# Kernel optimization log

Hardware: AMD Instinct MI355X
Metric: run time of the kernel (lower is better)

Reference implementation:

```python
import jax, jax.numpy as jnp
import numpy as np

EMBED = 1024
HEADS = 16
HEAD_DIM = EMBED // HEADS

def setup_inputs() -> dict:
    key = jax.random.key(0)
    k1, k2, k3, k4, k5 = jax.random.split(key, 5)
    scale = 1.0 / np.sqrt(EMBED)
    return {
        "x": jax.random.normal(k1, (4, 2048, EMBED), dtype=jnp.float32),
        "qkv_w": jax.random.uniform(k2, (3 * EMBED, EMBED), minval=-scale, maxval=scale, dtype=jnp.float32),
        "qkv_b": jax.random.uniform(k3, (3 * EMBED,), minval=-scale, maxval=scale, dtype=jnp.float32),
        "out_w": jax.random.uniform(k4, (EMBED, EMBED), minval=-scale, maxval=scale, dtype=jnp.float32),
        "out_b": jax.random.uniform(k5, (EMBED,), minval=-scale, maxval=scale, dtype=jnp.float32),
    }

def reference(x, qkv_w, qkv_b, out_w, out_b):
    b, n, _ = x.shape
    # torch Linear: x @ W.T + b
    qkv = (jnp.einsum('bne,fe->bnf', x, qkv_w) + qkv_b).reshape(b, n, 3, HEADS, HEAD_DIM)
    q, k, v = qkv[:, :, 0], qkv[:, :, 1], qkv[:, :, 2]
    scores = jnp.einsum('bnhd,bmhd->bhnm', q, k) / jnp.sqrt(jnp.float32(HEAD_DIM))
    attn = jax.nn.softmax(scores, axis=-1)  # dropout p=0.0 -> identity
    out = jnp.einsum('bhnm,bmhd->bnhd', attn, v).reshape(b, n, EMBED)
    return jnp.einsum('bne,fe->bnf', out, out_w) + out_b
```

## Files before the change

### kernel.cpp

```cpp
#include <hip/hip_runtime.h>
#include <hip/hip_bf16.h>

typedef __bf16 bf16;
typedef __attribute__((ext_vector_type(8))) __bf16 bf16x8;
typedef __attribute__((ext_vector_type(4))) __bf16 bf16x4;
typedef __attribute__((ext_vector_type(4))) float f32x4;
typedef __attribute__((ext_vector_type(16))) float f32x16;

#define EMBED 1024
#define HEADS 16
#define HD 64
#define NB 4
#define SEQ 2048
#define TOK (NB * SEQ)
#define F3 (3 * EMBED)

#define QSCALE 0.18033688011112042f
#define CEXP 16.0f

__device__ __forceinline__ float exp2_hw(float x) {
  float r;
  asm("v_exp_f32 %0, %1" : "=v"(r) : "v"(x));
  return r;
}

__device__ __forceinline__ unsigned int cvtpk_bf16(float lo, float hi) {
  unsigned int r;
  asm("v_cvt_pk_bf16_f32 %0, %1, %2" : "=v"(r) : "v"(lo), "v"(hi));
  return r;
}

__device__ __forceinline__ void gload_lds16(const void* g, void* l) {
  __builtin_amdgcn_global_load_lds(
      (const __attribute__((address_space(1))) unsigned int*)(unsigned long long)g,
      (__attribute__((address_space(3))) unsigned int*)(unsigned int)(unsigned long long)l,
      16, 0, 0);
}

__global__ void cvt_bf16_kernel(const float* __restrict__ in, bf16* __restrict__ out, int n4) {
  int i = blockIdx.x * blockDim.x + threadIdx.x;
  if (i < n4) {
    float4 v = ((const float4*)in)[i];
    bf16x4 o;
    o[0] = (bf16)v.x; o[1] = (bf16)v.y; o[2] = (bf16)v.z; o[3] = (bf16)v.w;
    ((bf16x4*)out)[i] = o;
  }
}

template <int MODE, typename OUT_T>
__global__ __launch_bounds__(256) void gemm_bt(const bf16* __restrict__ A,
                                               const bf16* __restrict__ Bw,
                                               const float* __restrict__ bias,
                                               OUT_T* __restrict__ C,
                                               bf16* __restrict__ VT,
                                               int K, int Ncols) {
  __shared__ __align__(16) bf16 As[2][128 * 32];
  __shared__ __align__(16) bf16 Bs[2][128 * 32];

  const int tid = threadIdx.x;
  const int lane = tid & 63;
  const int w = tid >> 6;
  const int wr = w >> 1, wc = w & 1;
  const int lr = lane & 15, lg = lane >> 4;

  const int r0 = tid >> 2;
  const int csw = ((tid & 3) ^ ((tid >> 3) & 3)) * 8;
  const bf16* Ag = A + (size_t)blockIdx.x * 128 * K + (size_t)r0 * K + csw;
  const bf16* Bg = Bw + (size_t)blockIdx.y * 128 * K + (size_t)r0 * K + csw;

  f32x4 acc[4][4] = {};
  const int co = (lg ^ ((lr >> 1) & 3)) * 8;
  const int ntiles = K >> 5;

#define GSTAGE(buf)                                      \
  do {                                                   \
    gload_lds16(Ag, &As[buf][tid * 8]);                  \
    gload_lds16(Ag + 64 * K, &As[buf][(tid + 256) * 8]); \
    gload_lds16(Bg, &Bs[buf][tid * 8]);                  \
    gload_lds16(Bg + 64 * K, &Bs[buf][(tid + 256) * 8]); \
    Ag += 32; Bg += 32;                                  \
  } while (0)

  GSTAGE(0);
  __syncthreads();

  for (int t = 0; t < ntiles; ++t) {
    const int cur = t & 1;
    if (t + 1 < ntiles) GSTAGE(cur ^ 1);

    bf16x8 af[4], bfr[4];
#pragma unroll
    for (int mi = 0; mi < 4; ++mi)
      af[mi] = *(const bf16x8*)&As[cur][(wr * 64 + mi * 16 + lr) * 32 + co];
#pragma unroll
    for (int ni = 0; ni < 4; ++ni)
      bfr[ni] = *(const bf16x8*)&Bs[cur][(wc * 64 + ni * 16 + lr) * 32 + co];

#pragma unroll
    for (int mi = 0; mi < 4; ++mi)
#pragma unroll
      for (int ni = 0; ni < 4; ++ni)
        acc[mi][ni] = __builtin_amdgcn_mfma_f32_16x16x32_bf16(af[mi], bfr[ni], acc[mi][ni], 0, 0, 0);

    __syncthreads();
  }
#undef GSTAGE

  const int rowb = blockIdx.x * 128 + wr * 64;
  const int colb = blockIdx.y * 128 + wc * 64;

  if (MODE == 1 && blockIdx.y >= 16) {
#pragma unroll
    for (int ni = 0; ni < 4; ++ni) {
      int col = colb + ni * 16 + lr;
      int fc = col - 2 * EMBED;
      int hh = fc >> 6, d = fc & 63;
      float bv = bias[col];
#pragma unroll
      for (int mi = 0; mi < 4; ++mi) {
        int row = rowb + mi * 16 + lg * 4;
        int bb = row >> 11, nn = row & 2047;
        bf16x4 pk;
#pragma unroll
        for (int j = 0; j < 4; ++j) pk[j] = (bf16)(acc[mi][ni][j] + bv);
        *(bf16x4*)&VT[((size_t)((bb * HEADS + hh) * HD + d)) * SEQ + nn] = pk;
      }
    }
  } else {
    const float scale = (MODE == 1 && blockIdx.y < 8) ? QSCALE : 1.0f;
#pragma unroll
    for (int ni = 0; ni < 4; ++ni) {
      int col = colb + ni * 16 + lr;
      float bv = bias[col];
#pragma unroll
      for (int mi = 0; mi < 4; ++mi) {
#pragma unroll
        for (int j = 0; j < 4; ++j) {
          int row = rowb + mi * 16 + lg * 4 + j;
          C[(size_t)row * Ncols + col] = (OUT_T)((acc[mi][ni][j] + bv) * scale);
        }
      }
    }
  }
}

__global__ __launch_bounds__(256, 4) void attn_fwd(const bf16* __restrict__ QK,
                                                   const bf16* __restrict__ VT,
                                                   bf16* __restrict__ O) {
  __shared__ __align__(16) bf16 Kb[2][64 * 64];
  __shared__ __align__(16) bf16 Vb[2][64 * 64];
  __shared__ float Lrow[4][32];

  const int qb = blockIdx.x, h = blockIdx.y, b = blockIdx.z;
  const int tid = threadIdx.x, lane = tid & 63, w = tid >> 6;
  const int lq = lane & 31, hi = lane >> 5;
  const int sw = lq & 7;

  bf16x8 qf[4];
  {
    const bf16* qp = QK + (size_t)(b * SEQ + qb * 128 + w * 32 + lq) * 2048 + h * HD + hi * 8;
#pragma unroll
    for (int c = 0; c < 4; ++c) qf[c] = *(const bf16x8*)(qp + c * 16);
  }

  const int rk = tid >> 3;
  const int cc = ((tid & 7) ^ (rk & 7)) * 8;
  const bf16* kp = QK + (size_t)(b * SEQ + rk) * 2048 + EMBED + h * HD + cc;
  const bf16* vp = VT + ((size_t)((b * HEADS + h) * HD + rk)) * SEQ + cc;

  f32x16 oacc[2] = {};
  float lp = 0.f;
  f32x16 cinit;
#pragma unroll
  for (int r = 0; r < 16; ++r) cinit[r] = -CEXP;

#define ASTAGE(buf)                                         \
  do {                                                      \
    gload_lds16(kp, &Kb[buf][tid * 8]);                     \
    gload_lds16(kp + 32 * 2048, &Kb[buf][(tid + 256) * 8]); \
    gload_lds16(vp, &Vb[buf][tid * 8]);                     \
    gload_lds16(vp + 32 * SEQ, &Vb[buf][(tid + 256) * 8]);  \
    kp += (size_t)64 * 2048; vp += 64;                      \
  } while (0)

  ASTAGE(0);
  __syncthreads();

  for (int t = 0; t < SEQ / 64; ++t) {
    const bf16* Kc = Kb[t & 1];
    const bf16* Vc = Vb[t & 1];
    if (t + 1 < SEQ / 64) ASTAGE((t & 1) ^ 1);

    f32x16 s0 = cinit, s1 = cinit;
    __builtin_amdgcn_s_setprio(1);
#pragma unroll
    for (int c = 0; c < 4; ++c) {
      const int cg = ((c * 2 + hi) ^ sw) * 8;
      bf16x8 kf0 = *(const bf16x8*)&Kc[lq * 64 + cg];
      bf16x8 kf1 = *(const bf16x8*)&Kc[(32 + lq) * 64 + cg];
      s0 = __builtin_amdgcn_mfma_f32_32x32x16_bf16(kf0, qf[c], s0, 0, 0, 0);
      s1 = __builtin_amdgcn_mfma_f32_32x32x16_bf16(kf1, qf[c], s1, 0, 0, 0);
    }
    __builtin_amdgcn_s_setprio(0);

    bf16x8 pa[4];
#pragma unroll
    for (int g = 0; g < 2; ++g) {
      const f32x16& sv = g ? s1 : s0;
      float pv[16];
#pragma unroll
      for (int r = 0; r < 16; ++r) { pv[r] = exp2_hw(sv[r]); lp += pv[r]; }
#pragma unroll
      for (int cidx = 0; cidx < 2; ++cidx) {
        const int pb = cidx * 8;
        unsigned int x0 = cvtpk_bf16(pv[pb + 0], pv[pb + 1]);
        unsigned int y0 = cvtpk_bf16(pv[pb + 4], pv[pb + 5]);
        unsigned int x1 = cvtpk_bf16(pv[pb + 2], pv[pb + 3]);
        unsigned int y1 = cvtpk_bf16(pv[pb + 6], pv[pb + 7]);
        auto r0 = __builtin_amdgcn_permlane32_swap(x0, y0, false, false);
        auto r1 = __builtin_amdgcn_permlane32_swap(x1, y1, false, false);
        union { unsigned int u[4]; bf16x8 v; } fr;
        fr.u[0] = r0[0]; fr.u[1] = r1[0]; fr.u[2] = r0[1]; fr.u[3] = r1[1];
        pa[g * 2 + cidx] = fr.v;
      }
    }

    __builtin_amdgcn_s_setprio(1);
#pragma unroll
    for (int k4 = 0; k4 < 4; ++k4) {
      const int cg = ((k4 * 2 + hi) ^ sw) * 8;
      bf16x8 vf0 = *(const bf16x8*)&Vc[lq * 64 + cg];
      bf16x8 vf1 = *(const bf16x8*)&Vc[(32 + lq) * 64 + cg];
      oacc[0] = __builtin_amdgcn_mfma_f32_32x32x16_bf16(pa[k4], vf0, oacc[0], 0, 0, 0);
      oacc[1] = __builtin_amdgcn_mfma_f32_32x32x16_bf16(pa[k4], vf1, oacc[1], 0, 0, 0);
    }
    __builtin_amdgcn_s_setprio(0);

    __syncthreads();
  }
#undef ASTAGE

  float lsum = lp + __shfl_xor(lp, 32, 64);
  if (hi == 0) Lrow[w][lq] = 1.0f / lsum;
  asm volatile("s_waitcnt lgkmcnt(0)" ::: "memory");

  const size_t obase = (size_t)(b * SEQ + qb * 128 + w * 32) * EMBED + h * HD + lq;
#pragma unroll
  for (int r = 0; r < 16; ++r) {
    const int qr = (r & 3) + 8 * (r >> 2) + 4 * hi;
    const float rl = Lrow[w][qr];
    O[obase + (size_t)qr * EMBED]      = (bf16)(oacc[0][r] * rl);
    O[obase + (size_t)qr * EMBED + 32] = (bf16)(oacc[1][r] * rl);
  }
}

extern "C" void kernel_launch(void* const* d_in, const int* in_sizes, int n_in,
                              void* d_out, int out_size, void* d_ws, size_t ws_size,
                              hipStream_t stream) {
  const float* x     = (const float*)d_in[0];
  const float* qkv_w = (const float*)d_in[1];
  const float* qkv_b = (const float*)d_in[2];
  const float* out_w = (const float*)d_in[3];
  const float* out_b = (const float*)d_in[4];
  float* out = (float*)d_out;

  char* ws = (char*)d_ws;
  bf16* xb    = (bf16*)(ws);
  bf16* wqb   = (bf16*)(ws + 16777216);
  bf16* wob   = (bf16*)(ws + 23068672);
  bf16* qk    = (bf16*)(ws + 25165824);
  bf16* vT    = (bf16*)(ws + 58720256);
  bf16* attno = (bf16*)(ws + 75497472);

  cvt_bf16_kernel<<<(TOK * EMBED / 4 + 255) / 256, 256, 0, stream>>>(x, xb, TOK * EMBED / 4);
  cvt_bf16_kernel<<<(F3 * EMBED / 4 + 255) / 256, 256, 0, stream>>>(qkv_w, wqb, F3 * EMBED / 4);
  cvt_bf16_kernel<<<(EMBED * EMBED / 4 + 255) / 256, 256, 0, stream>>>(out_w, wob, EMBED * EMBED / 4);

  gemm_bt<1, bf16><<<dim3(TOK / 128, F3 / 128), 256, 0, stream>>>(xb, wqb, qkv_b, qk, vT, EMBED, 2048);

  attn_fwd<<<dim3(SEQ / 128, HEADS, NB), 256, 0, stream>>>(qk, vT, attno);

  gemm_bt<0, float><<<dim3(TOK / 128, EMBED / 128), 256, 0, stream>>>(attno, wob, out_b, out, nullptr, EMBED, EMBED);
}
```

Baseline: 273.6 us.

## Process 256 queries per attention block with 64 rows per wave

Each wave of the attention kernel now handles two 32-row query groups, so every K and V tile staged in LDS and read into registers feeds twice as many MFMAs. The grid is halved to 512 blocks on a 1D launch, and the block index is remapped so that blocks with the same (batch, head) land on different XCDs or are spread in a particular order. Register pressure doubles for the accumulators, and launch bounds drop to 2 blocks per CU to fit. The fixed offset of the softmax exponent is unchanged.

```diff
diff --git a/kernel.cpp b/kernel.cpp
--- a/kernel.cpp
+++ b/kernel.cpp
@@ -144,23 +144,29 @@
   }
 }
 
-__global__ __launch_bounds__(256, 4) void attn_fwd(const bf16* __restrict__ QK,
+__global__ __launch_bounds__(256, 2) void attn_fwd(const bf16* __restrict__ QK,
                                                    const bf16* __restrict__ VT,
                                                    bf16* __restrict__ O) {
   __shared__ __align__(16) bf16 Kb[2][64 * 64];
   __shared__ __align__(16) bf16 Vb[2][64 * 64];
-  __shared__ float Lrow[4][32];
-
-  const int qb = blockIdx.x, h = blockIdx.y, b = blockIdx.z;
+  __shared__ float Lrow[4][64];
+
+  const int orig = blockIdx.x;
+  const int wid = ((orig & 7) << 6) | (orig >> 3);
+  const int qb = wid & 7;
+  const int g = wid >> 3;
+  const int h = g & 15, b = g >> 4;
+
   const int tid = threadIdx.x, lane = tid & 63, w = tid >> 6;
   const int lq = lane & 31, hi = lane >> 5;
   const int sw = lq & 7;
 
-  bf16x8 qf[4];
-  {
-    const bf16* qp = QK + (size_t)(b * SEQ + qb * 128 + w * 32 + lq) * 2048 + h * HD + hi * 8;
-#pragma unroll
-    for (int c = 0; c < 4; ++c) qf[c] = *(const bf16x8*)(qp + c * 16);
+  bf16x8 qf[2][4];
+#pragma unroll
+  for (int grp = 0; grp < 2; ++grp) {
+    const bf16* qp = QK + (size_t)(b * SEQ + qb * 256 + w * 64 + grp * 32 + lq) * 2048 + h * HD + hi * 8;
+#pragma unroll
+    for (int c = 0; c < 4; ++c) qf[grp][c] = *(const bf16x8*)(qp + c * 16);
   }
 
   const int rk = tid >> 3;
@@ -168,8 +174,8 @@
   const bf16* kp = QK + (size_t)(b * SEQ + rk) * 2048 + EMBED + h * HD + cc;
   const bf16* vp = VT + ((size_t)((b * HEADS + h) * HD + rk)) * SEQ + cc;
 
-  f32x16 oacc[2] = {};
-  float lp = 0.f;
+  f32x16 oacc[2][2] = {};
+  float lp0 = 0.f, lp1 = 0.f;
   f32x16 cinit;
 #pragma unroll
   for (int r = 0; r < 16; ++r) cinit[r] = -CEXP;
@@ -183,6 +189,25 @@
     kp += (size_t)64 * 2048; vp += 64;                      \
   } while (0)
 
+  auto packP = [&](const f32x16& sv, float& lpacc, bf16x8* pa) {
+    float pv[16];
+#pragma unroll
+    for (int r = 0; r < 16; ++r) { pv[r] = exp2_hw(sv[r]); lpacc += pv[r]; }
+#pragma unroll
+    for (int cidx = 0; cidx < 2; ++cidx) {
+      const int pb = cidx * 8;
+      unsigned int x0 = cvtpk_bf16(pv[pb + 0], pv[pb + 1]);
+      unsigned int y0 = cvtpk_bf16(pv[pb + 4], pv[pb + 5]);
+      unsigned int x1 = cvtpk_bf16(pv[pb + 2], pv[pb + 3]);
+      unsigned int y1 = cvtpk_bf16(pv[pb + 6], pv[pb + 7]);
+      auto r0 = __builtin_amdgcn_permlane32_swap(x0, y0, false, false);
+      auto r1 = __builtin_amdgcn_permlane32_swap(x1, y1, false, false);
+      union { unsigned int u[4]; bf16x8 v; } fr;
+      fr.u[0] = r0[0]; fr.u[1] = r1[0]; fr.u[2] = r0[1]; fr.u[3] = r1[1];
+      pa[cidx] = fr.v;
+    }
+  };
+
   ASTAGE(0);
   __syncthreads();
 
@@ -191,66 +216,61 @@
     const bf16* Vc = Vb[t & 1];
     if (t + 1 < SEQ / 64) ASTAGE((t & 1) ^ 1);
 
-    f32x16 s0 = cinit, s1 = cinit;
-    __builtin_amdgcn_s_setprio(1);
-#pragma unroll
-    for (int c = 0; c < 4; ++c) {
-      const int cg = ((c * 2 + hi) ^ sw) * 8;
-      bf16x8 kf0 = *(const bf16x8*)&Kc[lq * 64 + cg];
-      bf16x8 kf1 = *(const bf16x8*)&Kc[(32 + lq) * 64 + cg];
-      s0 = __builtin_amdgcn_mfma_f32_32x32x16_bf16(kf0, qf[c], s0, 0, 0, 0);
-      s1 = __builtin_amdgcn_mfma_f32_32x32x16_bf16(kf1, qf[c], s1, 0, 0, 0);
-    }
-    __builtin_amdgcn_s_setprio(0);
-
-    bf16x8 pa[4];
-#pragma unroll
-    for (int g = 0; g < 2; ++g) {
-      const f32x16& sv = g ? s1 : s0;
-      float pv[16];
-#pragma unroll
-      for (int r = 0; r < 16; ++r) { pv[r] = exp2_hw(sv[r]); lp += pv[r]; }
-#pragma unroll
-      for (int cidx = 0; cidx < 2; ++cidx) {
-        const int pb = cidx * 8;
-        unsigned int x0 = cvtpk_bf16(pv[pb + 0], pv[pb + 1]);
-        unsigned int y0 = cvtpk_bf16(pv[pb + 4], pv[pb + 5]);
-        unsigned int x1 = cvtpk_bf16(pv[pb + 2], pv[pb + 3]);
-        unsigned int y1 = cvtpk_bf16(pv[pb + 6], pv[pb + 7]);
-        auto r0 = __builtin_amdgcn_permlane32_swap(x0, y0, false, false);
-        auto r1 = __builtin_amdgcn_permlane32_swap(x1, y1, false, false);
-        union { unsigned int u[4]; bf16x8 v; } fr;
-        fr.u[0] = r0[0]; fr.u[1] = r1[0]; fr.u[2] = r0[1]; fr.u[3] = r1[1];
-        pa[g * 2 + cidx] = fr.v;
+#pragma unroll
+    for (int half = 0; half < 2; ++half) {
+      const int rbase = half * 32;
+
+      f32x16 s0 = cinit, s1 = cinit;
+      __builtin_amdgcn_s_setprio(1);
+#pragma unroll
+      for (int c = 0; c < 4; ++c) {
+        bf16x8 kf = *(const bf16x8*)&Kc[(rbase + lq) * 64 + ((c * 2 + hi) ^ sw) * 8];
+        s0 = __builtin_amdgcn_mfma_f32_32x32x16_bf16(kf, qf[0][c], s0, 0, 0, 0);
+        s1 = __builtin_amdgcn_mfma_f32_32x32x16_bf16(kf, qf[1][c], s1, 0, 0, 0);
       }
-    }
-
-    __builtin_amdgcn_s_setprio(1);
-#pragma unroll
-    for (int k4 = 0; k4 < 4; ++k4) {
-      const int cg = ((k4 * 2 + hi) ^ sw) * 8;
-      bf16x8 vf0 = *(const bf16x8*)&Vc[lq * 64 + cg];
-      bf16x8 vf1 = *(const bf16x8*)&Vc[(32 + lq) * 64 + cg];
-      oacc[0] = __builtin_amdgcn_mfma_f32_32x32x16_bf16(pa[k4], vf0, oacc[0], 0, 0, 0);
-      oacc[1] = __builtin_amdgcn_mfma_f32_32x32x16_bf16(pa[k4], vf1, oacc[1], 0, 0, 0);
-    }
-    __builtin_amdgcn_s_setprio(0);
+      __builtin_amdgcn_s_setprio(0);
+
+      bf16x8 pa0[2], pa1[2];
+      packP(s0, lp0, pa0);
+      packP(s1, lp1, pa1);
+
+      __builtin_amdgcn_s_setprio(1);
+#pragma unroll
+      for (int kl = 0; kl < 2; ++kl) {
+        const int k4 = half * 2 + kl;
+        const int cg = ((k4 * 2 + hi) ^ sw) * 8;
+        bf16x8 vf0 = *(const bf16x8*)&Vc[lq * 64 + cg];
+        bf16x8 vf1 = *(const bf16x8*)&Vc[(32 + lq) * 64 + cg];
+        oacc[0][0] = __builtin_amdgcn_mfma_f32_32x32x16_bf16(pa0[kl], vf0, oacc[0][0], 0, 0, 0);
+        oacc[0][1] = __builtin_amdgcn_mfma_f32_32x32x16_bf16(pa0[kl], vf1, oacc[0][1], 0, 0, 0);
+        oacc[1][0] = __builtin_amdgcn_mfma_f32_32x32x16_bf16(pa1[kl], vf0, oacc[1][0], 0, 0, 0);
+        oacc[1][1] = __builtin_amdgcn_mfma_f32_32x32x16_bf16(pa1[kl], vf1, oacc[1][1], 0, 0, 0);
+      }
+      __builtin_amdgcn_s_setprio(0);
+    }
 
     __syncthreads();
   }
 #undef ASTAGE
 
-  float lsum = lp + __shfl_xor(lp, 32, 64);
-  if (hi == 0) Lrow[w][lq] = 1.0f / lsum;
+  float ls0 = lp0 + __shfl_xor(lp0, 32, 64);
+  float ls1 = lp1 + __shfl_xor(lp1, 32, 64);
+  if (hi == 0) {
+    Lrow[w][lq] = 1.0f / ls0;
+    Lrow[w][32 + lq] = 1.0f / ls1;
+  }
   asm volatile("s_waitcnt lgkmcnt(0)" ::: "memory");
 
-  const size_t obase = (size_t)(b * SEQ + qb * 128 + w * 32) * EMBED + h * HD + lq;
-#pragma unroll
-  for (int r = 0; r < 16; ++r) {
-    const int qr = (r & 3) + 8 * (r >> 2) + 4 * hi;
-    const float rl = Lrow[w][qr];
-    O[obase + (size_t)qr * EMBED]      = (bf16)(oacc[0][r] * rl);
-    O[obase + (size_t)qr * EMBED + 32] = (bf16)(oacc[1][r] * rl);
+#pragma unroll
+  for (int grp = 0; grp < 2; ++grp) {
+    const size_t obase = (size_t)(b * SEQ + qb * 256 + w * 64 + grp * 32) * EMBED + h * HD + lq;
+#pragma unroll
+    for (int r = 0; r < 16; ++r) {
+      const int qr = (r & 3) + 8 * (r >> 2) + 4 * hi;
+      const float rl = Lrow[w][grp * 32 + qr];
+      O[obase + (size_t)qr * EMBED]      = (bf16)(oacc[grp][0][r] * rl);
+      O[obase + (size_t)qr * EMBED + 32] = (bf16)(oacc[grp][1][r] * rl);
+    }
   }
 }
 
@@ -278,7 +298,7 @@
 
   gemm_bt<1, bf16><<<dim3(TOK / 128, F3 / 128), 256, 0, stream>>>(xb, wqb, qkv_b, qk, vT, EMBED, 2048);
 
-  attn_fwd<<<dim3(SEQ / 128, HEADS, NB), 256, 0, stream>>>(qk, vT, attno);
+  attn_fwd<<<512, 256, 0, stream>>>(qk, vT, attno);
 
   gemm_bt<0, float><<<dim3(TOK / 128, EMBED / 128), 256, 0, stream>>>(attno, wob, out_b, out, nullptr, EMBED, EMBED);
 }
```

Result: faster. 256.2 us (-6.3%).
